# Performance work log

Hardware: AMD Instinct MI355X
Metric: run time of the kernel (lower is better)

Reference implementation:

```python
import jax, jax.numpy as jnp
import numpy as np

FEAT_DIM = 384
HEAD_DIM = 32
N_HEADS = FEAT_DIM // HEAD_DIM
MAX_SEQ_LEN = 64
SIZE = 8  # sqrt(max_seq_len)


def _get_relative_position_index(height, width):
    coords_h = np.arange(height)
    coords_w = np.arange(width)
    coords = np.stack(np.meshgrid(coords_h, coords_w, indexing='ij'))
    coords_flat = coords.reshape(coords.shape[0], -1)
    relative_coords = coords_flat[:, :, None] - coords_flat[:, None, :]
    relative_coords = relative_coords.transpose(1, 2, 0)
    rh = relative_coords[:, :, 0] + (height - 1)
    rw = relative_coords[:, :, 1] + (width - 1)
    return jnp.asarray(rh * (2 * width - 1) + rw, dtype=jnp.int32)  # [P, P]


def setup_inputs() -> dict:
    key = jax.random.key(0)
    ks = jax.random.split(key, 6)
    B, G, P, D = 32, 64, MAX_SEQ_LEN, FEAT_DIM
    x = jax.random.normal(ks[0], (B, G, P, D), dtype=jnp.float32)
    qkv_w = jax.random.normal(ks[1], (D, 3 * D), dtype=jnp.float32) * (1.0 / np.sqrt(D))
    qkv_b = jnp.zeros((3 * D,), dtype=jnp.float32)
    merge_w = jax.random.normal(ks[2], (D, D), dtype=jnp.float32) * (1.0 / np.sqrt(D))
    merge_b = jnp.zeros((D,), dtype=jnp.float32)
    n_bias = (2 * SIZE - 1) * (2 * SIZE - 1)  # 225
    bias_table = jax.random.truncated_normal(ks[3], -2.0, 2.0, (n_bias, N_HEADS), dtype=jnp.float32) * 0.02
    rel_index = _get_relative_position_index(SIZE, SIZE)
    return {"x": x, "qkv_w": qkv_w, "qkv_b": qkv_b, "merge_w": merge_w,
            "merge_b": merge_b, "bias_table": bias_table, "rel_index": rel_index}


def reference(x, qkv_w, qkv_b, merge_w, merge_b, bias_table, rel_index):
    B, G, P, D = x.shape
    H, DH = N_HEADS, HEAD_DIM
    scale = 1.0 / np.sqrt(D)  # NOTE: module scales by feat_dim**-0.5, not head_dim
    qkv = x @ qkv_w + qkv_b  # [B,G,P,3D]
    q, k, v = jnp.split(qkv, 3, axis=-1)
    q = q.reshape(B, G, P, H, DH).transpose(0, 1, 3, 2, 4)  # [B,G,H,P,DH]
    k = k.reshape(B, G, P, H, DH).transpose(0, 1, 3, 2, 4)
    v = v.reshape(B, G, P, H, DH).transpose(0, 1, 3, 2, 4)
    scores = jnp.einsum('bghid,bghjd->bghij', q, k * scale)  # [B,G,H,P,P]
    pos_bias = bias_table[rel_index.reshape(-1)].reshape(P, P, H)
    pos_bias = pos_bias.transpose(2, 0, 1)[None, None]  # [1,1,H,P,P]
    attn = jax.nn.softmax(scores + pos_bias, axis=-1)
    out = jnp.einsum('bghij,bghjd->bghid', attn, v)  # [B,G,H,P,DH]
    out = out.transpose(0, 1, 3, 2, 4).reshape(B, G, P, D)
    return out @ merge_w + merge_b
```

## Files before the change

### kernel.cpp

```cpp
#include <hip/hip_runtime.h>
#include <hip/hip_bf16.h>
#include <cstdint>
#include <cstddef>


typedef __bf16 bf16_t;
typedef __bf16 bf16x8 __attribute__((ext_vector_type(8)));
typedef float  f32x4  __attribute__((ext_vector_type(4)));

#define MFMA16(A, B, C) __builtin_amdgcn_mfma_f32_16x16x32_bf16((A), (B), (C), 0, 0, 0)

#define NBLK   2048
#define SCALE  0.051031036307982884f

#define XS   408
#define QKS  40
#define VTS  88
#define OFF_X 0
#define OFF_Q (64 * XS)
#define OFF_K (OFF_Q + 4 * 64 * QKS)
#define OFF_V (OFF_K + 4 * 64 * QKS)
#define OFF_P (OFF_V + 4 * 32 * VTS)
#define LDS_ELEMS (OFF_P + 8 * 32 * VTS)
#define LDS_BYTES (LDS_ELEMS * 2)

__global__ void prep_kernel(const float* __restrict__ qkv_w,
                            const float* __restrict__ qkv_b,
                            const float* __restrict__ merge_w,
                            const float* __restrict__ bias_table,
                            const int*   __restrict__ rel_index,
                            bf16_t* __restrict__ qkv_wT,
                            bf16_t* __restrict__ merge_wT,
                            float*  __restrict__ biasx,
                            float*  __restrict__ qkvb_s) {
  int idx = blockIdx.x * 256 + threadIdx.x;
  if (idx < 1152 * 384) {
    int n = idx / 384, k = idx - n * 384;
    float v = qkv_w[k * 1152 + n];
    if (n >= 384 && n < 768) v *= SCALE;
    qkv_wT[idx] = (bf16_t)v;
    return;
  }
  int i2 = idx - 1152 * 384;
  if (i2 < 384 * 384) {
    int n = i2 / 384, k = i2 - n * 384;
    merge_wT[i2] = (bf16_t)merge_w[k * 384 + n];
    return;
  }
  int i3 = i2 - 384 * 384;
  if (i3 < 12 * 64 * 64) {
    int h = i3 / 4096, r = i3 - h * 4096;
    biasx[i3] = bias_table[rel_index[r] * 12 + h];
    return;
  }
  int i4 = i3 - 12 * 64 * 64;
  if (i4 < 1152) {
    float v = qkv_b[i4];
    if (i4 >= 384 && i4 < 768) v *= SCALE;
    qkvb_s[i4] = v;
  }
}

__global__ void __launch_bounds__(512)
fused_qkv_attn(const float*  __restrict__ x,
               const bf16_t* __restrict__ wT,
               const float*  __restrict__ qbias,
               const float*  __restrict__ biasx,
               bf16_t* __restrict__ attn) {
  extern __shared__ char smem_raw[];
  bf16_t* lds = (bf16_t*)smem_raw;
  bf16_t* xs  = lds + OFF_X;
  bf16_t* qs  = lds + OFF_Q;
  bf16_t* ks  = lds + OFF_K;
  bf16_t* vts = lds + OFF_V;
  bf16_t* ps  = lds + OFF_P;

  const int tid  = threadIdx.x;
  const int blk  = blockIdx.x;
  const int lane = tid & 63;
  const int w    = tid >> 6;
  const int c    = lane & 15;
  const int g    = lane >> 4;

  const f32x4 zf = {0.f, 0.f, 0.f, 0.f};

  {
    const float4* xg = (const float4*)(x + (size_t)blk * (64 * 384));
#pragma unroll
    for (int it = 0; it < 12; ++it) {
      int idx = tid + it * 512;
      int row = idx / 96;
      int col = (idx - row * 96) * 4;
      float4 v = xg[idx];
      union { bf16_t b[4]; uint2 u; } pk;
      pk.b[0] = (bf16_t)v.x; pk.b[1] = (bf16_t)v.y;
      pk.b[2] = (bf16_t)v.z; pk.b[3] = (bf16_t)v.w;
      *(uint2*)(xs + row * XS + col) = pk.u;
    }
  }
  __syncthreads();

#pragma unroll 1
  for (int pass = 0; pass < 3; ++pass) {
    f32x4 acc[3][4];
#pragma unroll
    for (int t = 0; t < 3; ++t)
#pragma unroll
      for (int mt = 0; mt < 4; ++mt) acc[t][mt] = zf;

    int nrow[3];
    const bf16_t* wp[3];
#pragma unroll
    for (int t = 0; t < 3; ++t) {
      int tau  = w * 3 + t;
      int kind = tau >> 3;
      int u    = tau & 7;
      nrow[t]  = kind * 384 + (pass * 4 + (u >> 1)) * 32 + (u & 1) * 16;
      wp[t]    = wT + (size_t)(nrow[t] + c) * 384 + g * 8;
    }
    bf16x8 bc[3], bn[3];
#pragma unroll
    for (int t = 0; t < 3; ++t) bc[t] = *(const bf16x8*)(wp[t]);
#pragma unroll
    for (int k = 0; k < 12; ++k) {
      if (k < 11) {
#pragma unroll
        for (int t = 0; t < 3; ++t) bn[t] = *(const bf16x8*)(wp[t] + (k + 1) * 32);
      }
      bf16x8 a[4];
#pragma unroll
      for (int mt = 0; mt < 4; ++mt)
        a[mt] = *(const bf16x8*)(xs + (mt * 16 + c) * XS + k * 32 + g * 8);
#pragma unroll
      for (int t = 0; t < 3; ++t)
#pragma unroll
        for (int mt = 0; mt < 4; ++mt)
          acc[t][mt] = MFMA16(a[mt], bc[t], acc[t][mt]);
#pragma unroll
      for (int t = 0; t < 3; ++t) bc[t] = bn[t];
    }

    __syncthreads();

#pragma unroll
    for (int t = 0; t < 3; ++t) {
      int tau  = w * 3 + t;
      int kind = tau >> 3;
      int u    = tau & 7;
      int hl   = u >> 1, c16 = u & 1;
      float bv = qbias[nrow[t] + c];
      if (kind == 2) {
#pragma unroll
        for (int mt = 0; mt < 4; ++mt) {
          union { bf16_t b[4]; uint2 u2; } pk;
#pragma unroll
          for (int r = 0; r < 4; ++r) pk.b[r] = (bf16_t)(acc[t][mt][r] + bv);
          *(uint2*)(vts + (hl * 32 + c16 * 16 + c) * VTS + mt * 16 + g * 4) = pk.u2;
        }
      } else {
        bf16_t* dst = (kind == 0 ? qs : ks) + hl * 64 * QKS + c16 * 16 + c;
#pragma unroll
        for (int mt = 0; mt < 4; ++mt)
#pragma unroll
          for (int r = 0; r < 4; ++r)
            dst[(mt * 16 + g * 4 + r) * QKS] = (bf16_t)(acc[t][mt][r] + bv);
      }
    }
    __syncthreads();

    {
      const int hl = w >> 1, ih = w & 1;
      const int h  = pass * 4 + hl;

      f32x4 sacc[4][2];
#pragma unroll
      for (int mt = 0; mt < 4; ++mt)
#pragma unroll
        for (int nt = 0; nt < 2; ++nt) sacc[mt][nt] = zf;
      bf16x8 ka[4], qf[2];
#pragma unroll
      for (int mt = 0; mt < 4; ++mt)
        ka[mt] = *(const bf16x8*)(ks + (hl * 64 + mt * 16 + c) * QKS + g * 8);
#pragma unroll
      for (int nt = 0; nt < 2; ++nt)
        qf[nt] = *(const bf16x8*)(qs + (hl * 64 + ih * 32 + nt * 16 + c) * QKS + g * 8);
#pragma unroll
      for (int mt = 0; mt < 4; ++mt)
#pragma unroll
        for (int nt = 0; nt < 2; ++nt)
          sacc[mt][nt] = MFMA16(ka[mt], qf[nt], sacc[mt][nt]);

      const float* bp = biasx + h * 4096;
      float sv[4][2][4];
      float mx[2] = {-3.0e38f, -3.0e38f};
#pragma unroll
      for (int nt = 0; nt < 2; ++nt) {
        int i = ih * 32 + nt * 16 + c;
#pragma unroll
        for (int mt = 0; mt < 4; ++mt) {
          union { float4 v; float a[4]; } bb;
          bb.v = *(const float4*)(bp + i * 64 + mt * 16 + g * 4);
#pragma unroll
          for (int r = 0; r < 4; ++r) {
            float s = sacc[mt][nt][r] + bb.a[r];
            sv[mt][nt][r] = s;
            mx[nt] = fmaxf(mx[nt], s);
          }
        }
      }
#pragma unroll
      for (int nt = 0; nt < 2; ++nt) {
        mx[nt] = fmaxf(mx[nt], __shfl_xor(mx[nt], 16));
        mx[nt] = fmaxf(mx[nt], __shfl_xor(mx[nt], 32));
      }
      float l[2] = {0.f, 0.f};
#pragma unroll
      for (int nt = 0; nt < 2; ++nt)
#pragma unroll
        for (int mt = 0; mt < 4; ++mt)
#pragma unroll
          for (int r = 0; r < 4; ++r) {
            float p = exp2f((sv[mt][nt][r] - mx[nt]) * 1.4426950408889634f);
            sv[mt][nt][r] = p;
            l[nt] += p;
          }
#pragma unroll
      for (int nt = 0; nt < 2; ++nt) {
        l[nt] += __shfl_xor(l[nt], 16);
        l[nt] += __shfl_xor(l[nt], 32);
      }

#pragma unroll
      for (int nt = 0; nt < 2; ++nt)
#pragma unroll
        for (int mt = 0; mt < 4; ++mt) {
          union { bf16_t b[4]; uint2 u2; } pk;
#pragma unroll
          for (int r = 0; r < 4; ++r) pk.b[r] = (bf16_t)sv[mt][nt][r];
          *(uint2*)(ps + (w * 32 + nt * 16 + c) * VTS + mt * 16 + g * 4) = pk.u2;
        }

      f32x4 oacc[2][2];
#pragma unroll
      for (int m2 = 0; m2 < 2; ++m2)
#pragma unroll
        for (int nt = 0; nt < 2; ++nt) oacc[m2][nt] = zf;
#pragma unroll
      for (int kt = 0; kt < 2; ++kt) {
        bf16x8 va[2], pb[2];
#pragma unroll
        for (int m2 = 0; m2 < 2; ++m2)
          va[m2] = *(const bf16x8*)(vts + (hl * 32 + m2 * 16 + c) * VTS + kt * 32 + g * 8);
#pragma unroll
        for (int nt = 0; nt < 2; ++nt)
          pb[nt] = *(const bf16x8*)(ps + (w * 32 + nt * 16 + c) * VTS + kt * 32 + g * 8);
#pragma unroll
        for (int m2 = 0; m2 < 2; ++m2)
#pragma unroll
          for (int nt = 0; nt < 2; ++nt)
            oacc[m2][nt] = MFMA16(va[m2], pb[nt], oacc[m2][nt]);
      }

#pragma unroll
      for (int nt = 0; nt < 2; ++nt) {
        float inv = 1.0f / l[nt];
        int row = blk * 64 + ih * 32 + nt * 16 + c;
#pragma unroll
        for (int m2 = 0; m2 < 2; ++m2) {
          union { bf16_t b[4]; uint2 u2; } pk;
#pragma unroll
          for (int r = 0; r < 4; ++r) pk.b[r] = (bf16_t)(oacc[m2][nt][r] * inv);
          *(uint2*)(attn + (size_t)row * 384 + h * 32 + m2 * 16 + g * 4) = pk.u2;
        }
      }
    }
  }
}

__global__ void __launch_bounds__(512)
merge_gemm(const bf16_t* __restrict__ attn,
           const bf16_t* __restrict__ mwT,
           const float*  __restrict__ mb,
           float* __restrict__ out) {
  __shared__ bf16_t as[64 * XS];
  const int tid = threadIdx.x, blk = blockIdx.x;
  const int lane = tid & 63, w = tid >> 6, c = lane & 15, g = lane >> 4;

  {
    const int4* ag = (const int4*)(attn + (size_t)blk * (64 * 384));
#pragma unroll
    for (int it = 0; it < 6; ++it) {
      int idx = tid + it * 512;
      int row = idx / 48;
      int col = (idx - row * 48) * 8;
      *(int4*)(as + row * XS + col) = ag[idx];
    }
  }
  __syncthreads();

  const f32x4 zf = {0.f, 0.f, 0.f, 0.f};
  f32x4 acc[3][4];
#pragma unroll
  for (int t = 0; t < 3; ++t)
#pragma unroll
    for (int mt = 0; mt < 4; ++mt) acc[t][mt] = zf;

  const int n0 = w * 48;
  const bf16_t* wp[3];
#pragma unroll
  for (int t = 0; t < 3; ++t) wp[t] = mwT + (size_t)(n0 + t * 16 + c) * 384 + g * 8;
  bf16x8 bc[3], bn[3];
#pragma unroll
  for (int t = 0; t < 3; ++t) bc[t] = *(const bf16x8*)(wp[t]);
#pragma unroll
  for (int k = 0; k < 12; ++k) {
    if (k < 11) {
#pragma unroll
      for (int t = 0; t < 3; ++t) bn[t] = *(const bf16x8*)(wp[t] + (k + 1) * 32);
    }
    bf16x8 a[4];
#pragma unroll
    for (int mt = 0; mt < 4; ++mt)
      a[mt] = *(const bf16x8*)(as + (mt * 16 + c) * XS + k * 32 + g * 8);
#pragma unroll
    for (int t = 0; t < 3; ++t)
#pragma unroll
      for (int mt = 0; mt < 4; ++mt)
        acc[t][mt] = MFMA16(a[mt], bc[t], acc[t][mt]);
#pragma unroll
    for (int t = 0; t < 3; ++t) bc[t] = bn[t];
  }

#pragma unroll
  for (int t = 0; t < 3; ++t) {
    float bias = mb[n0 + t * 16 + c];
#pragma unroll
    for (int mt = 0; mt < 4; ++mt)
#pragma unroll
      for (int r = 0; r < 4; ++r)
        out[(size_t)(blk * 64 + mt * 16 + g * 4 + r) * 384 + n0 + t * 16 + c] =
            acc[t][mt][r] + bias;
  }
}

extern "C" void kernel_launch(void* const* d_in, const int* in_sizes, int n_in,
                              void* d_out, int out_size, void* d_ws, size_t ws_size,
                              hipStream_t stream) {
  const float* x          = (const float*)d_in[0];
  const float* qkv_w      = (const float*)d_in[1];
  const float* qkv_b      = (const float*)d_in[2];
  const float* merge_w    = (const float*)d_in[3];
  const float* merge_b    = (const float*)d_in[4];
  const float* bias_table = (const float*)d_in[5];
  const int*   rel_index  = (const int*)d_in[6];
  float*       out        = (float*)d_out;

  const size_t OFF_QKVWT = 0;
  const size_t OFF_MWT   = 884736;
  const size_t OFF_BIAS  = OFF_MWT + 294912;
  const size_t OFF_QB    = OFF_BIAS + 196608;
  const size_t OFF_ATTN  = OFF_QB + 4608;
  const size_t NEED      = OFF_ATTN + (size_t)100663296;
  if (ws_size < NEED) return;

  char* ws = (char*)d_ws;
  bf16_t* qkv_wT  = (bf16_t*)(ws + OFF_QKVWT);
  bf16_t* mwT     = (bf16_t*)(ws + OFF_MWT);
  float*  biasx   = (float*)(ws + OFF_BIAS);
  float*  qkvb_s  = (float*)(ws + OFF_QB);
  bf16_t* attnbuf = (bf16_t*)(ws + OFF_ATTN);

  prep_kernel<<<2501, 256, 0, stream>>>(qkv_w, qkv_b, merge_w, bias_table,
                                        rel_index, qkv_wT, mwT, biasx, qkvb_s);

  hipFuncSetAttribute(reinterpret_cast<const void*>(fused_qkv_attn),
                      hipFuncAttributeMaxDynamicSharedMemorySize, LDS_BYTES);
  fused_qkv_attn<<<NBLK, 512, LDS_BYTES, stream>>>(x, qkv_wT, qkvb_s, biasx, attnbuf);

  merge_gemm<<<NBLK, 512, 0, stream>>>(attnbuf, mwT, merge_b, out);
}
```

Baseline: 439.8 us.

## Shrink attention LDS by aliasing regions, XOR-swizzling, and reloading x per pass

Cuts the fused QKV+attention kernel's LDS footprint from about 140KB to 64KB. It aliases the Q buffer onto the x staging buffer, drops row padding in favour of XOR-swizzled 16-byte chunks, and reloads and reconverts x from global memory on each of the three passes. Launch bounds now request 4 waves per SIMD, so two 512-thread blocks can be resident per CU. The cost is three times the x global reads plus one extra barrier per pass, and tighter register limits that could cause spills.

```diff
diff --git a/kernel.cpp b/kernel.cpp
--- a/kernel.cpp
+++ b/kernel.cpp
@@ -13,16 +13,6 @@
 #define NBLK   2048
 #define SCALE  0.051031036307982884f
 
-#define XS   408
-#define QKS  40
-#define VTS  88
-#define OFF_X 0
-#define OFF_Q (64 * XS)
-#define OFF_K (OFF_Q + 4 * 64 * QKS)
-#define OFF_V (OFF_K + 4 * 64 * QKS)
-#define OFF_P (OFF_V + 4 * 32 * VTS)
-#define LDS_ELEMS (OFF_P + 8 * 32 * VTS)
-#define LDS_BYTES (LDS_ELEMS * 2)
 
 __global__ void prep_kernel(const float* __restrict__ qkv_w,
                             const float* __restrict__ qkv_b,
@@ -61,7 +51,7 @@
   }
 }
 
-__global__ void __launch_bounds__(512)
+__global__ void __launch_bounds__(512, 4)
 fused_qkv_attn(const float*  __restrict__ x,
                const bf16_t* __restrict__ wT,
                const float*  __restrict__ qbias,
@@ -69,11 +59,11 @@
                bf16_t* __restrict__ attn) {
   extern __shared__ char smem_raw[];
   bf16_t* lds = (bf16_t*)smem_raw;
-  bf16_t* xs  = lds + OFF_X;
-  bf16_t* qs  = lds + OFF_Q;
-  bf16_t* ks  = lds + OFF_K;
-  bf16_t* vts = lds + OFF_V;
-  bf16_t* ps  = lds + OFF_P;
+  bf16_t* xs  = lds;
+  bf16_t* qs  = lds;
+  bf16_t* ks  = lds + 8192;
+  bf16_t* vts = lds + 16384;
+  bf16_t* ps  = lds + 24576;
 
   const int tid  = threadIdx.x;
   const int blk  = blockIdx.x;
@@ -81,27 +71,31 @@
   const int w    = tid >> 6;
   const int c    = lane & 15;
   const int g    = lane >> 4;
+  const int cx   = c & 7;
 
   const f32x4 zf = {0.f, 0.f, 0.f, 0.f};
-
-  {
-    const float4* xg = (const float4*)(x + (size_t)blk * (64 * 384));
-#pragma unroll
-    for (int it = 0; it < 12; ++it) {
-      int idx = tid + it * 512;
-      int row = idx / 96;
-      int col = (idx - row * 96) * 4;
-      float4 v = xg[idx];
-      union { bf16_t b[4]; uint2 u; } pk;
-      pk.b[0] = (bf16_t)v.x; pk.b[1] = (bf16_t)v.y;
-      pk.b[2] = (bf16_t)v.z; pk.b[3] = (bf16_t)v.w;
-      *(uint2*)(xs + row * XS + col) = pk.u;
-    }
-  }
-  __syncthreads();
 
 #pragma unroll 1
   for (int pass = 0; pass < 3; ++pass) {
+    {
+      const float4* xg = (const float4*)(x + (size_t)blk * 24576);
+#pragma unroll
+      for (int it = 0; it < 6; ++it) {
+        int hc  = tid + it * 512;
+        int row = hc / 48;
+        int ch  = hc - row * 48;
+        float4 v0 = xg[hc * 2];
+        float4 v1 = xg[hc * 2 + 1];
+        union { bf16_t b[8]; uint4 u; } pk;
+        pk.b[0] = (bf16_t)v0.x; pk.b[1] = (bf16_t)v0.y;
+        pk.b[2] = (bf16_t)v0.z; pk.b[3] = (bf16_t)v0.w;
+        pk.b[4] = (bf16_t)v1.x; pk.b[5] = (bf16_t)v1.y;
+        pk.b[6] = (bf16_t)v1.z; pk.b[7] = (bf16_t)v1.w;
+        *(uint4*)(xs + row * 384 + ((ch ^ (row & 7)) << 3)) = pk.u;
+      }
+    }
+    __syncthreads();
+
     f32x4 acc[3][4];
 #pragma unroll
     for (int t = 0; t < 3; ++t)
@@ -128,9 +122,10 @@
         for (int t = 0; t < 3; ++t) bn[t] = *(const bf16x8*)(wp[t] + (k + 1) * 32);
       }
       bf16x8 a[4];
-#pragma unroll
-      for (int mt = 0; mt < 4; ++mt)
-        a[mt] = *(const bf16x8*)(xs + (mt * 16 + c) * XS + k * 32 + g * 8);
+      int chv = (((4 * k + g) ^ cx) << 3);
+#pragma unroll
+      for (int mt = 0; mt < 4; ++mt)
+        a[mt] = *(const bf16x8*)(xs + (mt * 16 + c) * 384 + chv);
 #pragma unroll
       for (int t = 0; t < 3; ++t)
 #pragma unroll
@@ -150,20 +145,23 @@
       int hl   = u >> 1, c16 = u & 1;
       float bv = qbias[nrow[t] + c];
       if (kind == 2) {
+        int d = c16 * 16 + c;
+        bf16_t* vbase = vts + hl * 2048 + d * 64;
 #pragma unroll
         for (int mt = 0; mt < 4; ++mt) {
           union { bf16_t b[4]; uint2 u2; } pk;
 #pragma unroll
           for (int r = 0; r < 4; ++r) pk.b[r] = (bf16_t)(acc[t][mt][r] + bv);
-          *(uint2*)(vts + (hl * 32 + c16 * 16 + c) * VTS + mt * 16 + g * 4) = pk.u2;
+          int chunk = (2 * mt + (g >> 1)) ^ cx;
+          *(uint2*)(vbase + chunk * 8 + (g & 1) * 4) = pk.u2;
         }
       } else {
-        bf16_t* dst = (kind == 0 ? qs : ks) + hl * 64 * QKS + c16 * 16 + c;
+        bf16_t* dst = (kind == 0 ? qs : ks) + hl * 2048 + c16 * 16 + c;
 #pragma unroll
         for (int mt = 0; mt < 4; ++mt)
 #pragma unroll
           for (int r = 0; r < 4; ++r)
-            dst[(mt * 16 + g * 4 + r) * QKS] = (bf16_t)(acc[t][mt][r] + bv);
+            dst[(mt * 16 + g * 4 + r) * 32] = (bf16_t)(acc[t][mt][r] + bv);
       }
     }
     __syncthreads();
@@ -180,10 +178,10 @@
       bf16x8 ka[4], qf[2];
 #pragma unroll
       for (int mt = 0; mt < 4; ++mt)
-        ka[mt] = *(const bf16x8*)(ks + (hl * 64 + mt * 16 + c) * QKS + g * 8);
+        ka[mt] = *(const bf16x8*)(ks + hl * 2048 + (mt * 16 + c) * 32 + g * 8);
 #pragma unroll
       for (int nt = 0; nt < 2; ++nt)
-        qf[nt] = *(const bf16x8*)(qs + (hl * 64 + ih * 32 + nt * 16 + c) * QKS + g * 8);
+        qf[nt] = *(const bf16x8*)(qs + hl * 2048 + (ih * 32 + nt * 16 + c) * 32 + g * 8);
 #pragma unroll
       for (int mt = 0; mt < 4; ++mt)
 #pragma unroll
@@ -230,35 +228,39 @@
         l[nt] += __shfl_xor(l[nt], 32);
       }
 
-#pragma unroll
-      for (int nt = 0; nt < 2; ++nt)
+      bf16_t* psw = ps + w * 1024;
+      bf16x8 va[2][2];
+#pragma unroll
+      for (int m2 = 0; m2 < 2; ++m2)
+#pragma unroll
+        for (int kt = 0; kt < 2; ++kt)
+          va[m2][kt] = *(const bf16x8*)(vts + hl * 2048 + (m2 * 16 + c) * 64 +
+                                        (((4 * kt + g) ^ cx) << 3));
+      f32x4 oacc[2][2];
+#pragma unroll
+      for (int m2 = 0; m2 < 2; ++m2)
+#pragma unroll
+        for (int nt = 0; nt < 2; ++nt) oacc[m2][nt] = zf;
+
+#pragma unroll
+      for (int nt = 0; nt < 2; ++nt) {
 #pragma unroll
         for (int mt = 0; mt < 4; ++mt) {
           union { bf16_t b[4]; uint2 u2; } pk;
 #pragma unroll
           for (int r = 0; r < 4; ++r) pk.b[r] = (bf16_t)sv[mt][nt][r];
-          *(uint2*)(ps + (w * 32 + nt * 16 + c) * VTS + mt * 16 + g * 4) = pk.u2;
+          int chunk = (2 * mt + (g >> 1)) ^ cx;
+          *(uint2*)(psw + c * 64 + chunk * 8 + (g & 1) * 4) = pk.u2;
         }
-
-      f32x4 oacc[2][2];
-#pragma unroll
-      for (int m2 = 0; m2 < 2; ++m2)
-#pragma unroll
-        for (int nt = 0; nt < 2; ++nt) oacc[m2][nt] = zf;
-#pragma unroll
-      for (int kt = 0; kt < 2; ++kt) {
-        bf16x8 va[2], pb[2];
+        bf16x8 pb[2];
+#pragma unroll
+        for (int kt = 0; kt < 2; ++kt)
+          pb[kt] = *(const bf16x8*)(psw + c * 64 + (((4 * kt + g) ^ cx) << 3));
 #pragma unroll
         for (int m2 = 0; m2 < 2; ++m2)
-          va[m2] = *(const bf16x8*)(vts + (hl * 32 + m2 * 16 + c) * VTS + kt * 32 + g * 8);
-#pragma unroll
-        for (int nt = 0; nt < 2; ++nt)
-          pb[nt] = *(const bf16x8*)(ps + (w * 32 + nt * 16 + c) * VTS + kt * 32 + g * 8);
-#pragma unroll
-        for (int m2 = 0; m2 < 2; ++m2)
-#pragma unroll
-          for (int nt = 0; nt < 2; ++nt)
-            oacc[m2][nt] = MFMA16(va[m2], pb[nt], oacc[m2][nt]);
+#pragma unroll
+          for (int kt = 0; kt < 2; ++kt)
+            oacc[m2][nt] = MFMA16(va[m2][kt], pb[kt], oacc[m2][nt]);
       }
 
 #pragma unroll
@@ -274,9 +276,11 @@
         }
       }
     }
+    __syncthreads();
   }
 }
 
+#define XS 408
 __global__ void __launch_bounds__(512)
 merge_gemm(const bf16_t* __restrict__ attn,
            const bf16_t* __restrict__ mwT,
@@ -374,8 +378,8 @@
                                         rel_index, qkv_wT, mwT, biasx, qkvb_s);
 
   hipFuncSetAttribute(reinterpret_cast<const void*>(fused_qkv_attn),
-                      hipFuncAttributeMaxDynamicSharedMemorySize, LDS_BYTES);
-  fused_qkv_attn<<<NBLK, 512, LDS_BYTES, stream>>>(x, qkv_wT, qkvb_s, biasx, attnbuf);
+                      hipFuncAttributeMaxDynamicSharedMemorySize, 65536);
+  fused_qkv_attn<<<NBLK, 512, 65536, stream>>>(x, qkv_wT, qkvb_s, biasx, attnbuf);
 
   merge_gemm<<<NBLK, 512, 0, stream>>>(attnbuf, mwT, merge_b, out);
 }
```

After: 504.1 us. 14.6% more time.
